# Performance work log

Hardware: AMD Instinct MI355X
Metric: run time of the kernel (lower is better)

The kernel has to match this reference:

```python
import jax, jax.numpy as jnp
import numpy as np

# Config derived from layers=[1024,1024,1024,1024,1024]
B = 16384      # batch
H1 = 1024      # layers[1], width of first odd layer (Ux target slice)
SE = 2048      # sum of even-layer dims (0 + 1024 + 1024)
SO = 2048      # sum of odd-layer dims (1024 + 1024)
LAYER = 1024
N_STEPS = 10


def rho(x):
    return jax.nn.sigmoid(4.0 * (x - 0.5))


def rhod(x):
    r = rho(x)
    return 4.0 * r * (1.0 - r)


def _block_mask():
    # Staircase blocks per layer_slices(): (0:1024,0:1024), (0:1024,1024:2048), (1024:2048,1024:2048)
    m = np.zeros((SE, SO), dtype=np.float32)
    m[0:LAYER, 0:LAYER] = 1.0
    m[0:LAYER, LAYER:2 * LAYER] = 1.0
    m[LAYER:2 * LAYER, LAYER:2 * LAYER] = 1.0
    return jnp.asarray(m)


def setup_inputs() -> dict:
    key = jax.random.key(0)
    k1, k2, k3, k4, k5 = jax.random.split(key, 5)
    Ux = jax.random.normal(k1, (B, H1), dtype=jnp.float32)
    s = jax.random.normal(k2, (B, SE + SO), dtype=jnp.float32)
    # Xavier uniform per 1024x1024 block: bound = sqrt(6 / (1024 + 1024))
    bound = (6.0 / (2 * LAYER)) ** 0.5
    W = jax.random.uniform(k3, (SE, SO), minval=-bound, maxval=bound, dtype=jnp.float32) * _block_mask()
    b_even = 0.01 * jax.random.normal(k4, (1, SE), dtype=jnp.float32)
    b_odd = 0.01 * jax.random.normal(k5, (1, SO), dtype=jnp.float32)
    return {"Ux": Ux, "s": s, "W": W, "b_even": b_even, "b_odd": b_odd}


def reference(Ux, s, W, b_even, b_odd):
    s_even, s_odd = s[:, :SE], s[:, SE:]
    # C_odd = rho(s_even) @ W + b_odd ; first odd layer also receives Ux
    C_odd = rho(s_even) @ W + b_odd
    C_odd = C_odd.at[:, :H1].add(Ux)
    for _ in range(N_STEPS):
        s_odd = 0.5 * s_odd + 0.5 * rhod(s_odd) * C_odd
    C_even = rho(s_odd) @ W.T + b_even
    for _ in range(N_STEPS):
        s_even = 0.5 * s_even + 0.5 * rhod(s_even) * C_even
    return jnp.concatenate([s_even, s_odd], axis=-1)
```

## Files before the change

kernel.cpp:

```cpp
#include <hip/hip_runtime.h>
#include <hip/hip_bf16.h>

#define BATCH 16384
#define SEW   2048
#define H1W   1024
#define NSTEP 10

typedef unsigned short u16;
typedef __attribute__((ext_vector_type(8))) __bf16 bf16x8;
typedef __attribute__((ext_vector_type(4))) float   f32x4;

__device__ __forceinline__ void split2(float x, u16& h, u16& l) {
    unsigned u = __float_as_uint(x);
    h = (u16)(u >> 16);
    float hf = __uint_as_float(u & 0xFFFF0000u);
    float r  = x - hf;
    l = (u16)(__float_as_uint(r) >> 16);
}

__device__ __forceinline__ float rho_f(float x) {
    return 1.0f / (1.0f + __expf(2.0f - 4.0f * x));
}

__device__ __forceinline__ void gl2lds16(const u16* g, u16* l) {
    __builtin_amdgcn_global_load_lds(
        (const __attribute__((address_space(1))) void*)g,
        (__attribute__((address_space(3))) void*)l, 16, 0, 0);
}

__global__ void prep_w(const float* __restrict__ W,
                       u16* __restrict__ Whi, u16* __restrict__ Wlo,
                       u16* __restrict__ WThi, u16* __restrict__ WTlo) {
    __shared__ float tile[32][33];
    const int tx = threadIdx.x, ty = threadIdx.y;
    const int x = blockIdx.x * 32 + tx;
#pragma unroll
    for (int k = 0; k < 4; ++k) {
        int y = blockIdx.y * 32 + ty + k * 8;
        float v = W[y * SEW + x];
        tile[ty + k * 8][tx] = v;
        u16 h, l; split2(v, h, l);
        Whi[y * SEW + x] = h; Wlo[y * SEW + x] = l;
    }
    __syncthreads();
#pragma unroll
    for (int k = 0; k < 4; ++k) {
        int r = blockIdx.x * 32 + ty + k * 8;
        int c = blockIdx.y * 32 + tx;
        float v = tile[tx][ty + k * 8];
        u16 h, l; split2(v, h, l);
        WThi[r * SEW + c] = h; WTlo[r * SEW + c] = l;
    }
}

__global__ void prep_rho(const float* __restrict__ s,
                         u16* __restrict__ Rhi, u16* __restrict__ Rlo) {
    int i = blockIdx.x * blockDim.x + threadIdx.x;
    int e = i << 2;
    int row = e >> 11;
    int col = e & 2047;
    const float4 v = *(const float4*)(s + ((size_t)row << 12) + col);
    float xs[4] = {v.x, v.y, v.z, v.w};
    u16 h[4], l[4];
#pragma unroll
    for (int k = 0; k < 4; ++k) {
        float r = rho_f(xs[k]);
        split2(r, h[k], l[k]);
    }
    *(ushort4*)(Rhi + e) = make_ushort4(h[0], h[1], h[2], h[3]);
    *(ushort4*)(Rlo + e) = make_ushort4(l[0], l[1], l[2], l[3]);
}

template <int PHASE>
__global__ __launch_bounds__(256, 3)
void gemm_fused(const u16* __restrict__ Ahi, const u16* __restrict__ Alo,
                const u16* __restrict__ Bhi, const u16* __restrict__ Blo,
                const float* __restrict__ bias,
                const float* __restrict__ Ux,
                const float* __restrict__ s_in,
                float* __restrict__ out,
                u16* __restrict__ R2hi, u16* __restrict__ R2lo) {
    __shared__ u16 ldsA[2][128 * 32];
    __shared__ u16 ldsB[2][128 * 32];

    const int tid = threadIdx.x;

    const int wg = blockIdx.x;
    const int L  = (wg & 7) * 256 + (wg >> 3);
    const int m0 = (L >> 4) * 128;
    const int n0 = (L & 15) * 128;

    int kt0, nkt;
    if (PHASE == 1) { kt0 = 0;                    nkt = (n0 < 1024) ? 32 : 64; }
    else            { kt0 = (n0 < 1024) ? 0 : 32; nkt = (n0 < 1024) ? 64 : 32; }
    const int nvt = 3 * nkt;

    const int srow = tid >> 2;
    const int sswz = (tid >> 3) & 3;
    const int scol = ((tid & 3) ^ sswz) * 8;
    const int aoff0 = (m0 + srow) * SEW + scol;
    const int boff0 = (n0 + srow) * SEW + scol;

    const int lane = tid & 63;
    const int w  = tid >> 6;
    const int wr = w >> 1, wc = w & 1;
    const int lr = lane & 15, q = lane >> 4;
    const int oh = ((q ^ ((lr >> 1) & 3))) << 4;
    int offA[4], offB[4];
#pragma unroll
    for (int i = 0; i < 4; ++i) {
        offA[i] = (wr * 64 + i * 16 + lr) * 64 + oh;
        offB[i] = (wc * 64 + i * 16 + lr) * 64 + oh;
    }

    f32x4 acc[4][4];
    const f32x4 zero = {0.f, 0.f, 0.f, 0.f};
#pragma unroll
    for (int i = 0; i < 4; ++i)
#pragma unroll
        for (int j = 0; j < 4; ++j) acc[i][j] = zero;

#define STAGE(As, Bs, kk, buf) do {                                          \
        u16* dA_ = &ldsA[buf][tid * 8];                                      \
        u16* dB_ = &ldsB[buf][tid * 8];                                      \
        const u16* sa_ = (As) + aoff0 + (kk);                                \
        const u16* sb_ = (Bs) + boff0 + (kk);                                \
        gl2lds16(sa_, dA_);                                                  \
        gl2lds16(sa_ + 64 * SEW, dA_ + 2048);                                \
        gl2lds16(sb_, dB_);                                                  \
        gl2lds16(sb_ + 64 * SEW, dB_ + 2048);                                \
    } while (0)

    int skk = kt0 * 32;
    int st  = 1;
    STAGE(Ahi, Bhi, skk, 0);

    for (int vt = 0; vt < nvt; ++vt) {
        const int cur = vt & 1;
        if (vt + 1 < nvt) {
            const u16* As = (st < 2)  ? Ahi : Alo;
            const u16* Bs = (st == 1) ? Blo : Bhi;
            STAGE(As, Bs, skk, cur ^ 1);
            if (++st == 3) { st = 0; skk += 32; }
            asm volatile("s_waitcnt vmcnt(4)" ::: "memory");
        } else {
            asm volatile("s_waitcnt vmcnt(0)" ::: "memory");
        }
        __builtin_amdgcn_s_barrier();

        const char* la = (const char*)ldsA[cur];
        const char* lb = (const char*)ldsB[cur];
        bf16x8 av[4], bv[4];
#pragma unroll
        for (int i = 0; i < 4; ++i) av[i] = *(const bf16x8*)(la + offA[i]);
#pragma unroll
        for (int j = 0; j < 4; ++j) bv[j] = *(const bf16x8*)(lb + offB[j]);

        __builtin_amdgcn_s_setprio(1);
#pragma unroll
        for (int i = 0; i < 4; ++i)
#pragma unroll
            for (int j = 0; j < 4; ++j)
                acc[i][j] = __builtin_amdgcn_mfma_f32_16x16x32_bf16(av[i], bv[j], acc[i][j], 0, 0, 0);
        __builtin_amdgcn_s_setprio(0);

        __builtin_amdgcn_s_barrier();
    }
#undef STAGE

#pragma unroll
    for (int i = 0; i < 4; ++i) {
#pragma unroll
        for (int j = 0; j < 4; ++j) {
            const int col = n0 + wc * 64 + j * 16 + lr;
            const float bvv = bias[col];
            float c[4], sv[4];
#pragma unroll
            for (int jj = 0; jj < 4; ++jj) {
                const int row = m0 + wr * 64 + i * 16 + q * 4 + jj;
                c[jj] = acc[i][j][jj] + bvv;
                if (PHASE == 1) {
                    if (n0 < 1024) c[jj] += Ux[(size_t)row * H1W + col];
                }
                sv[jj] = s_in[(size_t)row * 4096 + col];
            }
#pragma unroll 1
            for (int t = 0; t < NSTEP; ++t) {
#pragma unroll
                for (int jj = 0; jj < 4; ++jj) {
                    float r  = rho_f(sv[jj]);
                    float rd = 4.0f * r * (1.0f - r);
                    sv[jj] = 0.5f * sv[jj] + 0.5f * rd * c[jj];
                }
            }
#pragma unroll
            for (int jj = 0; jj < 4; ++jj) {
                const int row = m0 + wr * 64 + i * 16 + q * 4 + jj;
                out[(size_t)row * 4096 + col] = sv[jj];
                if (PHASE == 1) {
                    float r = rho_f(sv[jj]);
                    u16 h, l; split2(r, h, l);
                    R2hi[(size_t)row * SEW + col] = h;
                    R2lo[(size_t)row * SEW + col] = l;
                }
            }
        }
    }
}

extern "C" void kernel_launch(void* const* d_in, const int* in_sizes, int n_in,
                              void* d_out, int out_size, void* d_ws, size_t ws_size,
                              hipStream_t stream) {
    (void)in_sizes; (void)n_in; (void)out_size; (void)ws_size;
    const float* Ux     = (const float*)d_in[0];
    const float* s      = (const float*)d_in[1];
    const float* W      = (const float*)d_in[2];
    const float* b_even = (const float*)d_in[3];
    const float* b_odd  = (const float*)d_in[4];
    float* out = (float*)d_out;

    char* ws = (char*)d_ws;
    const size_t MB = 1024ull * 1024ull;
    u16* R1hi = (u16*)(ws);
    u16* R1lo = (u16*)(ws + 64 * MB);
    u16* R2hi = (u16*)(ws + 128 * MB);
    u16* R2lo = (u16*)(ws + 192 * MB);
    u16* Whi  = (u16*)(ws + 256 * MB);
    u16* Wlo  = (u16*)(ws + 264 * MB);
    u16* WThi = (u16*)(ws + 272 * MB);
    u16* WTlo = (u16*)(ws + 280 * MB);

    prep_w<<<dim3(64, 64), dim3(32, 8), 0, stream>>>(W, Whi, Wlo, WThi, WTlo);
    prep_rho<<<(BATCH * SEW / 4) / 256, 256, 0, stream>>>(s, R1hi, R1lo);

    gemm_fused<1><<<dim3(2048), 256, 0, stream>>>(
        R1hi, R1lo, WThi, WTlo, b_odd, Ux,
        s + SEW, out + SEW, R2hi, R2lo);

    gemm_fused<2><<<dim3(2048), 256, 0, stream>>>(
        R2hi, R2lo, Whi, Wlo, b_even, nullptr,
        s, out, nullptr, nullptr);
}
```

Measured before the change: 1.556 ms.

## Load hi/lo split tiles together per K-step to reuse operands across three MFMA passes

The K loop no longer runs three virtual tiles, each loading one hi/lo pairing. Each K-step now stages all four tiles (A hi/lo, B hi/lo) into separate LDS buffers once. The three bf16 MFMA product passes (hi*hi, hi*lo, lo*hi) then reuse the loaded fragments. This removes the redundant reloads of Ahi and Bhi and cuts barriers by three times, but doubles LDS use and raises register pressure, so occupancy is lowered from 3 to 2 blocks per CU.

```diff
diff --git a/kernel.cpp b/kernel.cpp
--- a/kernel.cpp
+++ b/kernel.cpp
@@ -72,7 +72,7 @@
 }
 
 template <int PHASE>
-__global__ __launch_bounds__(256, 3)
+__global__ __launch_bounds__(256, 2)
 void gemm_fused(const u16* __restrict__ Ahi, const u16* __restrict__ Alo,
                 const u16* __restrict__ Bhi, const u16* __restrict__ Blo,
                 const float* __restrict__ bias,
@@ -80,8 +80,10 @@
                 const float* __restrict__ s_in,
                 float* __restrict__ out,
                 u16* __restrict__ R2hi, u16* __restrict__ R2lo) {
-    __shared__ u16 ldsA[2][128 * 32];
-    __shared__ u16 ldsB[2][128 * 32];
+    __shared__ u16 lsAh[2][128 * 32];
+    __shared__ u16 lsAl[2][128 * 32];
+    __shared__ u16 lsBh[2][128 * 32];
+    __shared__ u16 lsBl[2][128 * 32];
 
     const int tid = threadIdx.x;
 
@@ -93,7 +95,6 @@
     int kt0, nkt;
     if (PHASE == 1) { kt0 = 0;                    nkt = (n0 < 1024) ? 32 : 64; }
     else            { kt0 = (n0 < 1024) ? 0 : 32; nkt = (n0 < 1024) ? 64 : 32; }
-    const int nvt = 3 * nkt;
 
     const int srow = tid >> 2;
     const int sswz = (tid >> 3) & 3;
@@ -120,51 +121,75 @@
 #pragma unroll
         for (int j = 0; j < 4; ++j) acc[i][j] = zero;
 
-#define STAGE(As, Bs, kk, buf) do {                                          \
-        u16* dA_ = &ldsA[buf][tid * 8];                                      \
-        u16* dB_ = &ldsB[buf][tid * 8];                                      \
-        const u16* sa_ = (As) + aoff0 + (kk);                                \
-        const u16* sb_ = (Bs) + boff0 + (kk);                                \
-        gl2lds16(sa_, dA_);                                                  \
-        gl2lds16(sa_ + 64 * SEW, dA_ + 2048);                                \
-        gl2lds16(sb_, dB_);                                                  \
-        gl2lds16(sb_ + 64 * SEW, dB_ + 2048);                                \
+#define STAGE(kk, buf) do {                                                  \
+        const int d0_ = tid * 8;                                             \
+        const u16* sa_ = Ahi + aoff0 + (kk);                                 \
+        const u16* sb_ = Bhi + boff0 + (kk);                                 \
+        const u16* sc_ = Alo + aoff0 + (kk);                                 \
+        const u16* sd_ = Blo + boff0 + (kk);                                 \
+        gl2lds16(sa_,            &lsAh[buf][d0_]);                           \
+        gl2lds16(sa_ + 64 * SEW, &lsAh[buf][d0_ + 2048]);                    \
+        gl2lds16(sb_,            &lsBh[buf][d0_]);                           \
+        gl2lds16(sb_ + 64 * SEW, &lsBh[buf][d0_ + 2048]);                    \
+        gl2lds16(sc_,            &lsAl[buf][d0_]);                           \
+        gl2lds16(sc_ + 64 * SEW, &lsAl[buf][d0_ + 2048]);                    \
+        gl2lds16(sd_,            &lsBl[buf][d0_]);                           \
+        gl2lds16(sd_ + 64 * SEW, &lsBl[buf][d0_ + 2048]);                    \
     } while (0)
 
-    int skk = kt0 * 32;
-    int st  = 1;
-    STAGE(Ahi, Bhi, skk, 0);
-
-    for (int vt = 0; vt < nvt; ++vt) {
-        const int cur = vt & 1;
-        if (vt + 1 < nvt) {
-            const u16* As = (st < 2)  ? Ahi : Alo;
-            const u16* Bs = (st == 1) ? Blo : Bhi;
-            STAGE(As, Bs, skk, cur ^ 1);
-            if (++st == 3) { st = 0; skk += 32; }
-            asm volatile("s_waitcnt vmcnt(4)" ::: "memory");
+    int kk = kt0 * 32;
+    STAGE(kk, 0);
+
+    for (int kt = 0; kt < nkt; ++kt) {
+        const int cur = kt & 1;
+        if (kt + 1 < nkt) {
+            STAGE(kk + 32, cur ^ 1);
+            asm volatile("s_waitcnt vmcnt(8)" ::: "memory");
         } else {
             asm volatile("s_waitcnt vmcnt(0)" ::: "memory");
         }
         __builtin_amdgcn_s_barrier();
 
-        const char* la = (const char*)ldsA[cur];
-        const char* lb = (const char*)ldsB[cur];
-        bf16x8 av[4], bv[4];
-#pragma unroll
-        for (int i = 0; i < 4; ++i) av[i] = *(const bf16x8*)(la + offA[i]);
-#pragma unroll
-        for (int j = 0; j < 4; ++j) bv[j] = *(const bf16x8*)(lb + offB[j]);
+        const char* pah = (const char*)lsAh[cur];
+        const char* pal = (const char*)lsAl[cur];
+        const char* pbh = (const char*)lsBh[cur];
+        const char* pbl = (const char*)lsBl[cur];
+        bf16x8 ah[4], al[4], bh[4], bl[4];
+#pragma unroll
+        for (int i = 0; i < 4; ++i) {
+            ah[i] = *(const bf16x8*)(pah + offA[i]);
+            bh[i] = *(const bf16x8*)(pbh + offB[i]);
+        }
+#pragma unroll
+        for (int i = 0; i < 4; ++i) {
+            al[i] = *(const bf16x8*)(pal + offA[i]);
+            bl[i] = *(const bf16x8*)(pbl + offB[i]);
+        }
 
         __builtin_amdgcn_s_setprio(1);
 #pragma unroll
         for (int i = 0; i < 4; ++i)
 #pragma unroll
             for (int j = 0; j < 4; ++j)
-                acc[i][j] = __builtin_amdgcn_mfma_f32_16x16x32_bf16(av[i], bv[j], acc[i][j], 0, 0, 0);
+                acc[i][j] = __builtin_amdgcn_mfma_f32_16x16x32_bf16(ah[i], bh[j], acc[i][j], 0, 0, 0);
         __builtin_amdgcn_s_setprio(0);
+        __builtin_amdgcn_s_setprio(1);
+#pragma unroll
+        for (int i = 0; i < 4; ++i)
+#pragma unroll
+            for (int j = 0; j < 4; ++j)
+                acc[i][j] = __builtin_amdgcn_mfma_f32_16x16x32_bf16(ah[i], bl[j], acc[i][j], 0, 0, 0);
+        __builtin_amdgcn_s_setprio(0);
+        __builtin_amdgcn_s_setprio(1);
+#pragma unroll
+        for (int i = 0; i < 4; ++i)
+#pragma unroll
+            for (int j = 0; j < 4; ++j)
+                acc[i][j] = __builtin_amdgcn_mfma_f32_16x16x32_bf16(al[i], bh[j], acc[i][j], 0, 0, 0);
+        __builtin_amdgcn_s_setprio(0);
 
         __builtin_amdgcn_s_barrier();
+        kk += 32;
     }
 #undef STAGE
 
```

Result: faster. 1.521 ms (-2.3%).
